# Kernel optimization log

Measured on AMD Instinct MI355X. Metric: run time of the kernel, lower is better.

Reference implementation:

```python
import jax, jax.numpy as jnp
import numpy as np

N = 50000
E = 1600000
IN_DIM = 256
HID = 64
OUT = 16
NEG_SLOPE = 0.01


def setup_inputs() -> dict:
    key = jax.random.key(0)
    ks = jax.random.split(key, 6)
    local_features = jax.random.normal(ks[0], (N, IN_DIM), dtype=jnp.float32)
    edge_index = jax.random.randint(ks[1], (2, E), 0, N, dtype=jnp.int32)
    W0 = jax.random.normal(ks[2], (IN_DIM, HID), dtype=jnp.float32) * 0.05
    a0 = jax.random.normal(ks[3], (2 * HID, 1), dtype=jnp.float32) * 0.05
    W1 = jax.random.normal(ks[4], (HID, OUT), dtype=jnp.float32) * 0.05
    a1 = jax.random.normal(ks[5], (2 * OUT, 1), dtype=jnp.float32) * 0.05
    return {"local_features": local_features, "edge_index": edge_index,
            "W0": W0, "a0": a0, "W1": W1, "a1": a1}


def _segment_softmax(scores, seg, num_segments):
    # softmax over edges sharing the same row (destination) id
    smax = jax.ops.segment_max(scores, seg, num_segments=num_segments)
    ex = jnp.exp(scores - smax[seg])
    ssum = jax.ops.segment_sum(ex, seg, num_segments=num_segments)
    return ex / ssum[seg]


def _gat_layer(H, row, col, W, a, apply_elu):
    d = W.shape[1]
    Hw = H @ W                                   # [N, d]
    # score_e = leaky_relu([Hw[row] || Hw[col]] @ a) = leaky_relu(pr[row] + pc[col])
    pr = Hw @ a[:d, 0]                           # [N]
    pc = Hw @ a[d:, 0]                           # [N]
    s = pr[row] + pc[col]                        # [E]
    s = jnp.where(s >= 0, s, NEG_SLOPE * s)      # leaky_relu
    att = _segment_softmax(s, row, Hw.shape[0])  # per-row sparse softmax (dim=1)
    # out[row] = sum_e att_e * Hw[col_e]
    out = jax.ops.segment_sum(att[:, None] * Hw[col], row, num_segments=Hw.shape[0])
    if apply_elu:
        out = jnp.where(out > 0, out, jnp.expm1(out))  # elu
    return out


def reference(local_features, edge_index, W0, a0, W1, a1):
    row = edge_index[0]
    col = edge_index[1]
    H = _gat_layer(local_features, row, col, W0, a0, apply_elu=True)
    H = _gat_layer(H, row, col, W1, a1, apply_elu=False)
    return jax.nn.log_softmax(H, axis=1)
```

## Files before the change

### kernel.cpp

```cpp
#include <hip/hip_runtime.h>
#include <hip/hip_bf16.h>
#include <math.h>

#define NN 50000
#define NE 1600000
#define BSH 7
#define BCK 391
#define BCAP 5120
#define GEMM_BLKS 98

typedef __attribute__((ext_vector_type(8))) short bf16x8;
typedef __attribute__((ext_vector_type(4))) float f32x4;
typedef __attribute__((ext_vector_type(2))) float f32x2;

__device__ __forceinline__ short f2bf(float f) {
    return (short)((__float_as_uint(f) + 0x8000u) >> 16);
}
__device__ __forceinline__ float lo16(unsigned u) { return __uint_as_float(u << 16); }
__device__ __forceinline__ float hi16(unsigned u) { return __uint_as_float(u & 0xffff0000u); }
__device__ __forceinline__ unsigned enc_f(float f) {
    unsigned u = __float_as_uint(f);
    return (u & 0x80000000u) ? ~u : (u | 0x80000000u);
}
__device__ __forceinline__ float dec_f(unsigned e) {
    return (e & 0x80000000u) ? __uint_as_float(e & 0x7FFFFFFFu)
                             : __uint_as_float(~e);
}

__global__ void __launch_bounds__(1024) gbinA_kernel(
        const float* __restrict__ X,
        const float* __restrict__ W0,
        const float* __restrict__ a,
        __hip_bfloat16* __restrict__ Hwb,
        float* __restrict__ pr,
        float* __restrict__ pc,
        unsigned* __restrict__ max0,
        const int* __restrict__ row, const int* __restrict__ col,
        int* __restrict__ gcursor, unsigned* __restrict__ staging) {
    __shared__ union SH {
        struct {
            unsigned lds_stage[8192];
            unsigned lds_addr[8192];
            int lds_cnt[512];
            int lds_off[512];
            int wg_goff[512];
            int wtot[8];
        } a;
        struct {
            ushort Wt[64 * 264];
            unsigned bmax;
        } g;
    } sh;
    int tid = threadIdx.x;

    if (blockIdx.x < GEMM_BLKS) {
        if (tid == 0) sh.g.bmax = 0u;
        for (int i = tid; i < 16384; i += 1024)
            sh.g.Wt[(i & 63) * 264 + (i >> 6)] = (ushort)f2bf(W0[i]);
        __syncthreads();
        int g256 = tid >> 8, t256 = tid & 255;
        int lane = t256 & 63, wid = t256 >> 6;
        int c = lane & 15, quad = lane >> 4;
        const ushort* wtp[4];
#pragma unroll
        for (int g = 0; g < 4; ++g) wtp[g] = &sh.g.Wt[(g * 16 + c) * 264 + quad * 8];
        float aA[4], aB[4];
#pragma unroll
        for (int g = 0; g < 4; ++g) { aA[g] = a[g * 16 + c]; aB[g] = a[64 + g * 16 + c]; }

        int row0 = blockIdx.x * 512 + g256 * 128 + wid * 16;
        float qmax = -1e30f;

#pragma unroll
        for (int tt = 0; tt < 2; ++tt) {
            int rt = row0 + tt * 64;
            int arow = rt + c; if (arow >= NN) arow = NN - 1;
            const float* xbase = X + (size_t)arow * 256 + quad * 8;
            f32x4 acc[4];
#pragma unroll
            for (int g = 0; g < 4; ++g) acc[g] = (f32x4){0.f, 0.f, 0.f, 0.f};

#pragma unroll
            for (int k0 = 0; k0 < 256; k0 += 32) {
                float4 xa = *(const float4*)(xbase + k0);
                float4 xb = *(const float4*)(xbase + k0 + 4);
                bf16x8 af;
                af[0] = f2bf(xa.x); af[1] = f2bf(xa.y); af[2] = f2bf(xa.z); af[3] = f2bf(xa.w);
                af[4] = f2bf(xb.x); af[5] = f2bf(xb.y); af[6] = f2bf(xb.z); af[7] = f2bf(xb.w);
#pragma unroll
                for (int g = 0; g < 4; ++g) {
                    bf16x8 bg = *(const bf16x8*)(wtp[g] + k0);
                    acc[g] = __builtin_amdgcn_mfma_f32_16x16x32_bf16(af, bg, acc[g], 0, 0, 0);
                }
            }

#pragma unroll
            for (int r = 0; r < 4; ++r) {
                int rr = rt + quad * 4 + r;
                float v0 = acc[0][r], v1 = acc[1][r], v2 = acc[2][r], v3 = acc[3][r];
                if (rr < NN) {
                    __hip_bfloat16* hp = Hwb + (size_t)rr * 64 + c;
                    hp[0]  = __float2bfloat16(v0);
                    hp[16] = __float2bfloat16(v1);
                    hp[32] = __float2bfloat16(v2);
                    hp[48] = __float2bfloat16(v3);
                }
                float pv = v0 * aA[0] + v1 * aA[1] + v2 * aA[2] + v3 * aA[3];
                float qv = v0 * aB[0] + v1 * aB[1] + v2 * aB[2] + v3 * aB[3];
#pragma unroll
                for (int off = 8; off; off >>= 1) {
                    pv += __shfl_xor(pv, off);
                    qv += __shfl_xor(qv, off);
                }
                if (c == 0 && rr < NN) { pr[rr] = pv; pc[rr] = qv; }
                if (rr < NN) qmax = fmaxf(qmax, qv);
            }
        }
        qmax = fmaxf(qmax, __shfl_xor(qmax, 16));
        qmax = fmaxf(qmax, __shfl_xor(qmax, 32));
        if (lane == 0) atomicMax(&sh.g.bmax, enc_f(qmax));
        __syncthreads();
        if (tid == 0) atomicMax(max0, sh.g.bmax);
        return;
    }

    int t = tid;
    int lane = t & 63;
    int w = t >> 6;
    int nbin = gridDim.x - GEMM_BLKS;

    for (int cb = (blockIdx.x - GEMM_BLKS) * 8192; cb < NE; cb += nbin * 8192) {
        int cnt_edges = NE - cb; if (cnt_edges > 8192) cnt_edges = 8192;
        if (t < 512) sh.a.lds_cnt[t] = 0;
        __syncthreads();
        int myb[8]; int mylo[8]; unsigned mypk[8];
        int e0 = cb + t * 8;
        if (t * 8 + 7 < cnt_edges) {
            int4 r0 = *(const int4*)(row + e0);
            int4 r1 = *(const int4*)(row + e0 + 4);
            int4 c0 = *(const int4*)(col + e0);
            int4 c1 = *(const int4*)(col + e0 + 4);
            int rr[8] = {r0.x, r0.y, r0.z, r0.w, r1.x, r1.y, r1.z, r1.w};
            int cc[8] = {c0.x, c0.y, c0.z, c0.w, c1.x, c1.y, c1.z, c1.w};
            #pragma unroll
            for (int i = 0; i < 8; ++i) {
                int b = rr[i] >> BSH;
                myb[i] = b;
                mypk[i] = ((unsigned)(rr[i] & 127) << 16) | (unsigned)cc[i];
                mylo[i] = atomicAdd(&sh.a.lds_cnt[b], 1);
            }
        } else {
            #pragma unroll
            for (int i = 0; i < 8; ++i) {
                int idx = t * 8 + i;
                myb[i] = -1;
                if (idx < cnt_edges) {
                    int e = cb + idx;
                    int r = row[e], c = col[e];
                    myb[i] = r >> BSH;
                    mypk[i] = ((unsigned)(r & 127) << 16) | (unsigned)c;
                    mylo[i] = atomicAdd(&sh.a.lds_cnt[myb[i]], 1);
                }
            }
        }
        __syncthreads();
        int v = (t < 512) ? sh.a.lds_cnt[t] : 0;
        int x = v;
        #pragma unroll
        for (int off = 1; off < 64; off <<= 1) {
            int y = __shfl_up(x, off);
            if (lane >= off) x += y;
        }
        if (t < 512 && lane == 63) sh.a.wtot[w] = x;
        __syncthreads();
        if (t < 8) {
            int s = sh.a.wtot[t];
            #pragma unroll
            for (int off = 1; off < 8; off <<= 1) {
                int y = __shfl_up(s, off, 8);
                if ((t & 7) >= off) s += y;
            }
            sh.a.wtot[t] = s;
        }
        __syncthreads();
        if (t < 512) {
            int add = (w > 0) ? sh.a.wtot[w - 1] : 0;
            sh.a.lds_off[t] = x - v + add;
        }
        if (t < BCK) {
            int cc2 = sh.a.lds_cnt[t];
            sh.a.wg_goff[t] = t * BCAP + (cc2 ? atomicAdd(&gcursor[t], cc2) : 0);
        }
        __syncthreads();
        #pragma unroll
        for (int i = 0; i < 8; ++i) if (myb[i] >= 0) {
            int p = sh.a.lds_off[myb[i]] + mylo[i];
            sh.a.lds_stage[p] = mypk[i];
            sh.a.lds_addr[p] = (unsigned)(sh.a.wg_goff[myb[i]] + mylo[i]);
        }
        __syncthreads();
        for (int i = t; i < cnt_edges; i += 1024)
            staging[sh.a.lds_addr[i]] = sh.a.lds_stage[i];
        __syncthreads();
    }
}

__global__ void __launch_bounds__(1024) binB_kernel(
        const int* __restrict__ gcursor,
        const unsigned* __restrict__ staging,
        int* __restrict__ rowptr,
        ushort* __restrict__ colperm) {
    __shared__ int bsc[512];
    __shared__ int bw[8];
    __shared__ int cur[128];
    __shared__ int wls2[2];
    __shared__ ushort lds_col[BCAP];
    int b = blockIdx.x;
    int t = threadIdx.x;
    int lane = t & 63;
    int w = t >> 6;

    if (t < 512) {
        int v = 0;
        if (t < BCK) {
            v = gcursor[t];
            if (v > BCAP) v = BCAP;
        }
        int x = v;
        #pragma unroll
        for (int off = 1; off < 64; off <<= 1) {
            int y = __shfl_up(x, off);
            if (lane >= off) x += y;
        }
        if (lane == 63) bw[w] = x;
        bsc[t] = x - v;
    }
    __syncthreads();
    if (t < 8) {
        int s = bw[t];
        #pragma unroll
        for (int off = 1; off < 8; off <<= 1) {
            int y = __shfl_up(s, off, 8);
            if ((t & 7) >= off) s += y;
        }
        bw[t] = s;
    }
    __syncthreads();
    int gbase = bsc[b] + ((b >= 64) ? bw[(b >> 6) - 1] : 0);
    int cnt = gcursor[b];
    if (cnt > BCAP) cnt = BCAP;
    if (b == 0 && t == 0) rowptr[NN] = bw[7];
    int rbase = b << BSH;
    int nrows = NN - rbase; if (nrows > 128) nrows = 128;
    const unsigned* sb = staging + (size_t)b * BCAP;

    unsigned ev[8];
    #pragma unroll
    for (int j = 0; j < 2; ++j) {
        int i0 = t * 4 + j * 4096;
        uint4 val = {0u, 0u, 0u, 0u};
        if (i0 + 3 < cnt) {
            val = *(const uint4*)(sb + i0);
        } else {
            if (i0 + 0 < cnt) val.x = sb[i0 + 0];
            if (i0 + 1 < cnt) val.y = sb[i0 + 1];
            if (i0 + 2 < cnt) val.z = sb[i0 + 2];
            if (i0 + 3 < cnt) val.w = sb[i0 + 3];
        }
        ev[j * 4 + 0] = val.x; ev[j * 4 + 1] = val.y;
        ev[j * 4 + 2] = val.z; ev[j * 4 + 3] = val.w;
    }

    if (t < 128) cur[t] = 0;
    __syncthreads();
    #pragma unroll
    for (int j = 0; j < 2; ++j) {
        #pragma unroll
        for (int l = 0; l < 4; ++l) {
            int idx = t * 4 + j * 4096 + l;
            if (idx < cnt) atomicAdd(&cur[ev[j * 4 + l] >> 16], 1);
        }
    }
    __syncthreads();
    int v = 0, x = 0;
    if (t < 128) {
        v = cur[t];
        x = v;
        #pragma unroll
        for (int off = 1; off < 64; off <<= 1) {
            int y = __shfl_up(x, off);
            if (lane >= off) x += y;
        }
        if (lane == 63) wls2[w] = x;
    }
    __syncthreads();
    int excl = 0;
    if (t < 128) {
        excl = x - v + ((w == 1) ? wls2[0] : 0);
        if (t < nrows) rowptr[rbase + t] = gbase + excl;
    }
    __syncthreads();
    if (t < 128) cur[t] = excl;
    __syncthreads();
    #pragma unroll
    for (int j = 0; j < 2; ++j) {
        #pragma unroll
        for (int l = 0; l < 4; ++l) {
            int idx = t * 4 + j * 4096 + l;
            if (idx < cnt) {
                unsigned e = ev[j * 4 + l];
                int pos = atomicAdd(&cur[e >> 16], 1);
                lds_col[pos] = (ushort)(e & 0xFFFFu);
            }
        }
    }
    __syncthreads();
    for (int i = t; i < cnt; i += 1024)
        colperm[gbase + i] = lds_col[i];
}

__global__ void __launch_bounds__(256) node0_kernel(
        const int* __restrict__ rowptr,
        const ushort* __restrict__ colperm,
        const float* __restrict__ pr,
        const float* __restrict__ pc,
        const unsigned* __restrict__ pcmax,
        const ushort* __restrict__ Hwb,
        const float* __restrict__ W1,
        const float* __restrict__ a1,
        __hip_bfloat16* __restrict__ Hw1b,
        float* __restrict__ pr1,
        float* __restrict__ pc1,
        unsigned* __restrict__ max1s) {
    __shared__ float W1s[64 * 17];
    __shared__ float a1s[32];
    __shared__ float hbuf[4][64];
    __shared__ unsigned long long wcbuf[4][64];
    __shared__ unsigned bmax1;
    int t = threadIdx.x;
    if (t == 0) bmax1 = 0u;
    for (int i = t; i < 64 * 16; i += 256)
        W1s[(i >> 4) * 17 + (i & 15)] = W1[i];
    if (t < 32) a1s[t] = a1[t];
    __syncthreads();

    int lane = t & 63;
    int wid = t >> 6;
    int node = blockIdx.x * 4 + wid;
    int k = lane & 15, q = lane >> 4;
    int start = rowptr[node], end = rowptr[node + 1];
    float pri = pr[node];
    float m = pri + dec_f(*pcmax);
    m = (m >= 0.f) ? m : 0.01f * m;

    float wsum = 0.f;
    f32x2 accA = {0.f, 0.f}, accB = {0.f, 0.f};
    for (int base = start; base < end; base += 64) {
        int n = end - base; if (n > 64) n = 64;
        float wv = 0.f; unsigned cv = 0;
        if (lane < n) {
            cv = (unsigned)colperm[base + lane];
            float s = pri + pc[cv];
            s = (s >= 0.f) ? s : 0.01f * s;
            wv = __expf(s - m);
        }
        wsum += wv;
        wcbuf[wid][lane] = ((unsigned long long)cv << 32) |
                           (unsigned long long)__float_as_uint(wv);
        int iters = (n + 3) >> 2;
        #pragma unroll 4
        for (int jj = 0; jj < iters; ++jj) {
            unsigned long long wc = wcbuf[wid][jj * 4 + q];
            float wj = __uint_as_float((unsigned)wc);
            int cj = (int)(wc >> 32);
            uint2 hv = *(const uint2*)(Hwb + (size_t)cj * 64 + k * 4);
            f32x2 wj2 = {wj, wj};
            f32x2 h01 = {lo16(hv.x), hi16(hv.x)};
            f32x2 h23 = {lo16(hv.y), hi16(hv.y)};
            accA += wj2 * h01;
            accB += wj2 * h23;
        }
    }
#pragma unroll
    for (int off = 32; off; off >>= 1) wsum += __shfl_xor(wsum, off);
    float acc0 = accA.x, acc1 = accA.y, acc2 = accB.x, acc3 = accB.y;
    acc0 += __shfl_xor(acc0, 16); acc0 += __shfl_xor(acc0, 32);
    acc1 += __shfl_xor(acc1, 16); acc1 += __shfl_xor(acc1, 32);
    acc2 += __shfl_xor(acc2, 16); acc2 += __shfl_xor(acc2, 32);
    acc3 += __shfl_xor(acc3, 16); acc3 += __shfl_xor(acc3, 32);

    float inv = (wsum > 0.f) ? 1.f / wsum : 0.f;
    float h0 = acc0 * inv; h0 = (h0 > 0.f) ? h0 : (__expf(h0) - 1.f);
    float h1 = acc1 * inv; h1 = (h1 > 0.f) ? h1 : (__expf(h1) - 1.f);
    float h2 = acc2 * inv; h2 = (h2 > 0.f) ? h2 : (__expf(h2) - 1.f);
    float h3 = acc3 * inv; h3 = (h3 > 0.f) ? h3 : (__expf(h3) - 1.f);
    if (q == 0) {
        float4 hh = {h0, h1, h2, h3};
        *(float4*)&hbuf[wid][k * 4] = hh;
    }
    int j = lane & 15, p = lane >> 4;
    const float* hbp = hbuf[wid];
    float vj = 0.f;
#pragma unroll
    for (int i = 0; i < 16; ++i) {
        int kk = p * 16 + i;
        vj = fmaf(hbp[kk], W1s[kk * 17 + j], vj);
    }
    vj += __shfl_xor(vj, 16);
    vj += __shfl_xor(vj, 32);
    if (p == 0) Hw1b[(size_t)node * 16 + j] = __float2bfloat16(vj);
    float pv = vj * a1s[j];
    float qv = vj * a1s[16 + j];
#pragma unroll
    for (int off = 8; off; off >>= 1) {
        pv += __shfl_xor(pv, off);
        qv += __shfl_xor(qv, off);
    }
    if (lane == 0) {
        pr1[node] = pv; pc1[node] = qv;
        atomicMax(&bmax1, enc_f(qv));
    }
    __syncthreads();
    if (t == 0) atomicMax(&max1s[(blockIdx.x & 31) * 16], bmax1);
}

__global__ void __launch_bounds__(256) node1_kernel(
        const int* __restrict__ rowptr,
        const ushort* __restrict__ colperm,
        const float* __restrict__ pr,
        const float* __restrict__ pc,
        const unsigned* __restrict__ max1s,
        const ushort* __restrict__ Hwb,
        float* __restrict__ out) {
    __shared__ unsigned long long wcbuf[4][64];
    __shared__ unsigned gmx;
    int t = threadIdx.x;
    if (t < 32) {
        unsigned v = max1s[t * 16];
        #pragma unroll
        for (int off = 16; off; off >>= 1) {
            unsigned o = (unsigned)__shfl_xor((int)v, off, 32);
            v = (v > o) ? v : o;
        }
        if (t == 0) gmx = v;
    }
    __syncthreads();
    int lane = t & 63;
    int wid = t >> 6;
    int node = blockIdx.x * 4 + wid;
    int k = lane & 3, q = lane >> 2;
    int start = rowptr[node], end = rowptr[node + 1];
    float pri = pr[node];
    float m = pri + dec_f(gmx);
    m = (m >= 0.f) ? m : 0.01f * m;

    float wsum = 0.f;
    f32x2 accA = {0.f, 0.f}, accB = {0.f, 0.f};
    for (int base = start; base < end; base += 64) {
        int n = end - base; if (n > 64) n = 64;
        float wv = 0.f; unsigned cv = 0;
        if (lane < n) {
            cv = (unsigned)colperm[base + lane];
            float s = pri + pc[cv];
            s = (s >= 0.f) ? s : 0.01f * s;
            wv = __expf(s - m);
        }
        wsum += wv;
        wcbuf[wid][lane] = ((unsigned long long)cv << 32) |
                           (unsigned long long)__float_as_uint(wv);
        int iters = (n + 15) >> 4;
        #pragma unroll 4
        for (int jj = 0; jj < iters; ++jj) {
            unsigned long long wc = wcbuf[wid][jj * 16 + q];
            float wj = __uint_as_float((unsigned)wc);
            int cj = (int)(wc >> 32);
            uint2 hv = *(const uint2*)(Hwb + (size_t)cj * 16 + k * 4);
            f32x2 wj2 = {wj, wj};
            accA += wj2 * (f32x2){lo16(hv.x), hi16(hv.x)};
            accB += wj2 * (f32x2){lo16(hv.y), hi16(hv.y)};
        }
    }
#pragma unroll
    for (int off = 32; off; off >>= 1) wsum += __shfl_xor(wsum, off);
    float ac[4] = {accA.x, accA.y, accB.x, accB.y};
#pragma unroll
    for (int j4 = 0; j4 < 4; ++j4) {
        ac[j4] += __shfl_xor(ac[j4], 4);
        ac[j4] += __shfl_xor(ac[j4], 8);
        ac[j4] += __shfl_xor(ac[j4], 16);
        ac[j4] += __shfl_xor(ac[j4], 32);
    }
    float inv = (wsum > 0.f) ? 1.f / wsum : 0.f;
    float v0 = ac[0] * inv, v1 = ac[1] * inv;
    float v2 = ac[2] * inv, v3 = ac[3] * inv;
    float mm = fmaxf(fmaxf(v0, v1), fmaxf(v2, v3));
    mm = fmaxf(mm, __shfl_xor(mm, 1, 4));
    mm = fmaxf(mm, __shfl_xor(mm, 2, 4));
    float ssx = __expf(v0 - mm) + __expf(v1 - mm) + __expf(v2 - mm) + __expf(v3 - mm);
    ssx += __shfl_xor(ssx, 1, 4);
    ssx += __shfl_xor(ssx, 2, 4);
    float lse = mm + __logf(ssx);
    if (q == 0) {
        float4 o = {v0 - lse, v1 - lse, v2 - lse, v3 - lse};
        *(float4*)(out + (size_t)node * 16 + k * 4) = o;
    }
}

extern "C" void kernel_launch(void* const* d_in, const int* in_sizes, int n_in,
                              void* d_out, int out_size, void* d_ws, size_t ws_size,
                              hipStream_t stream) {
    const float* X  = (const float*)d_in[0];
    const int*   ei = (const int*)d_in[1];
    const float* W0 = (const float*)d_in[2];
    const float* a0 = (const float*)d_in[3];
    const float* W1 = (const float*)d_in[4];
    const float* a1 = (const float*)d_in[5];
    float* out = (float*)d_out;

    const int* row = ei;
    const int* col = ei + NE;

    char* wsb = (char*)d_ws;
    size_t off = 0;
    auto alloc = [&](size_t bytes) {
        void* p = wsb + off;
        off += (bytes + 15) & ~(size_t)15;
        return p;
    };
    unsigned* maxes = (unsigned*)alloc(16);
    unsigned* max1s = (unsigned*)alloc(512 * 4);
    int* gcursor    = (int*)alloc(512 * 4);
    size_t zinit = off;
    int* rowptr     = (int*)alloc((NN + 2) * 4);
    unsigned* staging = (unsigned*)alloc((size_t)BCK * BCAP * 4);
    ushort* colperm = (ushort*)alloc((size_t)NE * 2);
    __hip_bfloat16* Hw0b = (__hip_bfloat16*)alloc((size_t)NN * 64 * 2);
    float* pr0      = (float*)alloc(NN * 4);
    float* pc0      = (float*)alloc(NN * 4);
    __hip_bfloat16* Hw1b = (__hip_bfloat16*)alloc((size_t)NN * 16 * 2);
    float* pr1      = (float*)alloc(NN * 4);
    float* pc1      = (float*)alloc(NN * 4);

    hipMemsetAsync(wsb, 0, zinit, stream);

    gbinA_kernel<<<GEMM_BLKS + 196, 1024, 0, stream>>>(X, W0, a0, Hw0b, pr0, pc0,
                                                       &maxes[0], row, col,
                                                       gcursor, staging);
    binB_kernel<<<BCK, 1024, 0, stream>>>(gcursor, staging, rowptr, colperm);

    node0_kernel<<<NN / 4, 256, 0, stream>>>(rowptr, colperm, pr0, pc0,
                                             &maxes[0], (const ushort*)Hw0b,
                                             W1, a1, Hw1b, pr1, pc1, max1s);

    node1_kernel<<<NN / 4, 256, 0, stream>>>(rowptr, colperm, pr1, pc1,
                                             max1s, (const ushort*)Hw1b, out);
}
```

Measured before the change: 206.0 us.

## Split layer-0 aggregation into two column-range passes for cache locality

Edges in each row are binned by whether their column index falls below or above a split point, and a mid pointer per row is recorded. Layer-0 aggregation is split into two kernels, each gathering features from only half the node range, so the gathered working set is smaller and more cache-resident. Partial accumulators and weight sums from the first pass go through a large global buffer that the second pass reads back. This adds a full extra launch plus substantial extra memory traffic for the intermediate accumulators.

```diff
diff --git a/kernel.cpp b/kernel.cpp
--- a/kernel.cpp
+++ b/kernel.cpp
@@ -8,6 +8,7 @@
 #define BCK 391
 #define BCAP 5120
 #define GEMM_BLKS 98
+#define COLSPLIT 25000
 
 typedef __attribute__((ext_vector_type(8))) short bf16x8;
 typedef __attribute__((ext_vector_type(4))) float f32x4;
@@ -209,11 +210,12 @@
         const int* __restrict__ gcursor,
         const unsigned* __restrict__ staging,
         int* __restrict__ rowptr,
+        int* __restrict__ midptr,
         ushort* __restrict__ colperm) {
     __shared__ int bsc[512];
     __shared__ int bw[8];
-    __shared__ int cur[128];
-    __shared__ int wls2[2];
+    __shared__ int cur[256];
+    __shared__ int wls4[4];
     __shared__ ushort lds_col[BCAP];
     int b = blockIdx.x;
     int t = threadIdx.x;
@@ -271,36 +273,7 @@
         ev[j * 4 + 2] = val.z; ev[j * 4 + 3] = val.w;
     }
 
-    if (t < 128) cur[t] = 0;
-    __syncthreads();
-    #pragma unroll
-    for (int j = 0; j < 2; ++j) {
-        #pragma unroll
-        for (int l = 0; l < 4; ++l) {
-            int idx = t * 4 + j * 4096 + l;
-            if (idx < cnt) atomicAdd(&cur[ev[j * 4 + l] >> 16], 1);
-        }
-    }
-    __syncthreads();
-    int v = 0, x = 0;
-    if (t < 128) {
-        v = cur[t];
-        x = v;
-        #pragma unroll
-        for (int off = 1; off < 64; off <<= 1) {
-            int y = __shfl_up(x, off);
-            if (lane >= off) x += y;
-        }
-        if (lane == 63) wls2[w] = x;
-    }
-    __syncthreads();
-    int excl = 0;
-    if (t < 128) {
-        excl = x - v + ((w == 1) ? wls2[0] : 0);
-        if (t < nrows) rowptr[rbase + t] = gbase + excl;
-    }
-    __syncthreads();
-    if (t < 128) cur[t] = excl;
+    if (t < 256) cur[t] = 0;
     __syncthreads();
     #pragma unroll
     for (int j = 0; j < 2; ++j) {
@@ -309,7 +282,51 @@
             int idx = t * 4 + j * 4096 + l;
             if (idx < cnt) {
                 unsigned e = ev[j * 4 + l];
-                int pos = atomicAdd(&cur[e >> 16], 1);
+                int bin = (int)((e >> 16) << 1) | (int)((e & 0xffffu) >= COLSPLIT);
+                atomicAdd(&cur[bin], 1);
+            }
+        }
+    }
+    __syncthreads();
+    int v = 0, x = 0;
+    if (t < 256) {
+        v = cur[t];
+        x = v;
+        #pragma unroll
+        for (int off = 1; off < 64; off <<= 1) {
+            int y = __shfl_up(x, off);
+            if (lane >= off) x += y;
+        }
+        if (lane == 63) wls4[w] = x;
+    }
+    __syncthreads();
+    if (t == 0) {
+        int s = 0;
+        #pragma unroll
+        for (int i = 0; i < 4; ++i) { int tv = wls4[i]; wls4[i] = s; s += tv; }
+    }
+    __syncthreads();
+    int excl = 0;
+    if (t < 256) {
+        excl = x - v + wls4[w];
+        int r = t >> 1;
+        if (r < nrows) {
+            if ((t & 1) == 0) rowptr[rbase + r] = gbase + excl;
+            else              midptr[rbase + r] = gbase + excl;
+        }
+    }
+    __syncthreads();
+    if (t < 256) cur[t] = excl;
+    __syncthreads();
+    #pragma unroll
+    for (int j = 0; j < 2; ++j) {
+        #pragma unroll
+        for (int l = 0; l < 4; ++l) {
+            int idx = t * 4 + j * 4096 + l;
+            if (idx < cnt) {
+                unsigned e = ev[j * 4 + l];
+                int bin = (int)((e >> 16) << 1) | (int)((e & 0xffffu) >= COLSPLIT);
+                int pos = atomicAdd(&cur[bin], 1);
                 lds_col[pos] = (ushort)(e & 0xFFFFu);
             }
         }
@@ -319,13 +336,71 @@
         colperm[gbase + i] = lds_col[i];
 }
 
-__global__ void __launch_bounds__(256) node0_kernel(
+__global__ void __launch_bounds__(256) node0a_kernel(
         const int* __restrict__ rowptr,
+        const int* __restrict__ midptr,
         const ushort* __restrict__ colperm,
         const float* __restrict__ pr,
         const float* __restrict__ pc,
         const unsigned* __restrict__ pcmax,
         const ushort* __restrict__ Hwb,
+        float* __restrict__ accbuf,
+        float* __restrict__ wsumA) {
+    __shared__ unsigned long long wcbuf[4][64];
+    int t = threadIdx.x;
+    int lane = t & 63;
+    int wid = t >> 6;
+    int node = blockIdx.x * 4 + wid;
+    int k = lane & 15, q = lane >> 4;
+    int start = rowptr[node], end = midptr[node];
+    float pri = pr[node];
+    float m = pri + dec_f(*pcmax);
+    m = (m >= 0.f) ? m : 0.01f * m;
+
+    float wsum = 0.f;
+    f32x2 accA = {0.f, 0.f}, accB = {0.f, 0.f};
+    for (int base = start; base < end; base += 64) {
+        int n = end - base; if (n > 64) n = 64;
+        float wv = 0.f; unsigned cv = 0;
+        if (lane < n) {
+            cv = (unsigned)colperm[base + lane];
+            float s = pri + pc[cv];
+            s = (s >= 0.f) ? s : 0.01f * s;
+            wv = __expf(s - m);
+        }
+        wsum += wv;
+        wcbuf[wid][lane] = ((unsigned long long)cv << 32) |
+                           (unsigned long long)__float_as_uint(wv);
+        int iters = (n + 3) >> 2;
+        #pragma unroll 4
+        for (int jj = 0; jj < iters; ++jj) {
+            unsigned long long wc = wcbuf[wid][jj * 4 + q];
+            float wj = __uint_as_float((unsigned)wc);
+            int cj = (int)(wc >> 32);
+            uint2 hv = *(const uint2*)(Hwb + (size_t)cj * 64 + k * 4);
+            f32x2 wj2 = {wj, wj};
+            accA += wj2 * (f32x2){lo16(hv.x), hi16(hv.x)};
+            accB += wj2 * (f32x2){lo16(hv.y), hi16(hv.y)};
+        }
+    }
+#pragma unroll
+    for (int off = 32; off; off >>= 1) wsum += __shfl_xor(wsum, off);
+    if (lane == 0) wsumA[node] = wsum;
+    f32x4 av = {accA.x, accA.y, accB.x, accB.y};
+    __builtin_nontemporal_store(av,
+        (f32x4*)(accbuf + ((size_t)node << 8) + lane * 4));
+}
+
+__global__ void __launch_bounds__(256) node0b_kernel(
+        const int* __restrict__ rowptr,
+        const int* __restrict__ midptr,
+        const ushort* __restrict__ colperm,
+        const float* __restrict__ pr,
+        const float* __restrict__ pc,
+        const unsigned* __restrict__ pcmax,
+        const ushort* __restrict__ Hwb,
+        const float* __restrict__ accbuf,
+        const float* __restrict__ wsumA,
         const float* __restrict__ W1,
         const float* __restrict__ a1,
         __hip_bfloat16* __restrict__ Hw1b,
@@ -348,13 +423,15 @@
     int wid = t >> 6;
     int node = blockIdx.x * 4 + wid;
     int k = lane & 15, q = lane >> 4;
-    int start = rowptr[node], end = rowptr[node + 1];
+    int start = midptr[node], end = rowptr[node + 1];
     float pri = pr[node];
     float m = pri + dec_f(*pcmax);
     m = (m >= 0.f) ? m : 0.01f * m;
 
+    f32x4 av = __builtin_nontemporal_load(
+        (const f32x4*)(accbuf + ((size_t)node << 8) + lane * 4));
+    f32x2 accA = {av.x, av.y}, accB = {av.z, av.w};
     float wsum = 0.f;
-    f32x2 accA = {0.f, 0.f}, accB = {0.f, 0.f};
     for (int base = start; base < end; base += 64) {
         int n = end - base; if (n > 64) n = 64;
         float wv = 0.f; unsigned cv = 0;
@@ -375,14 +452,13 @@
             int cj = (int)(wc >> 32);
             uint2 hv = *(const uint2*)(Hwb + (size_t)cj * 64 + k * 4);
             f32x2 wj2 = {wj, wj};
-            f32x2 h01 = {lo16(hv.x), hi16(hv.x)};
-            f32x2 h23 = {lo16(hv.y), hi16(hv.y)};
-            accA += wj2 * h01;
-            accB += wj2 * h23;
+            accA += wj2 * (f32x2){lo16(hv.x), hi16(hv.x)};
+            accB += wj2 * (f32x2){lo16(hv.y), hi16(hv.y)};
         }
     }
 #pragma unroll
     for (int off = 32; off; off >>= 1) wsum += __shfl_xor(wsum, off);
+    wsum += wsumA[node];
     float acc0 = accA.x, acc1 = accA.y, acc2 = accB.x, acc3 = accB.y;
     acc0 += __shfl_xor(acc0, 16); acc0 += __shfl_xor(acc0, 32);
     acc1 += __shfl_xor(acc1, 16); acc1 += __shfl_xor(acc1, 32);
@@ -532,6 +608,7 @@
     int* gcursor    = (int*)alloc(512 * 4);
     size_t zinit = off;
     int* rowptr     = (int*)alloc((NN + 2) * 4);
+    int* midptr     = (int*)alloc((NN + 2) * 4);
     unsigned* staging = (unsigned*)alloc((size_t)BCK * BCAP * 4);
     ushort* colperm = (ushort*)alloc((size_t)NE * 2);
     __hip_bfloat16* Hw0b = (__hip_bfloat16*)alloc((size_t)NN * 64 * 2);
@@ -540,17 +617,23 @@
     __hip_bfloat16* Hw1b = (__hip_bfloat16*)alloc((size_t)NN * 16 * 2);
     float* pr1      = (float*)alloc(NN * 4);
     float* pc1      = (float*)alloc(NN * 4);
+    float* accbuf   = (float*)alloc((size_t)NN * 256 * 4);
+    float* wsumA    = (float*)alloc(NN * 4);
 
     hipMemsetAsync(wsb, 0, zinit, stream);
 
     gbinA_kernel<<<GEMM_BLKS + 196, 1024, 0, stream>>>(X, W0, a0, Hw0b, pr0, pc0,
                                                        &maxes[0], row, col,
                                                        gcursor, staging);
-    binB_kernel<<<BCK, 1024, 0, stream>>>(gcursor, staging, rowptr, colperm);
-
-    node0_kernel<<<NN / 4, 256, 0, stream>>>(rowptr, colperm, pr0, pc0,
-                                             &maxes[0], (const ushort*)Hw0b,
-                                             W1, a1, Hw1b, pr1, pc1, max1s);
+    binB_kernel<<<BCK, 1024, 0, stream>>>(gcursor, staging, rowptr, midptr, colperm);
+
+    node0a_kernel<<<NN / 4, 256, 0, stream>>>(rowptr, midptr, colperm, pr0, pc0,
+                                              &maxes[0], (const ushort*)Hw0b,
+                                              accbuf, wsumA);
+    node0b_kernel<<<NN / 4, 256, 0, stream>>>(rowptr, midptr, colperm, pr0, pc0,
+                                              &maxes[0], (const ushort*)Hw0b,
+                                              accbuf, wsumA,
+                                              W1, a1, Hw1b, pr1, pc1, max1s);
 
     node1_kernel<<<NN / 4, 256, 0, stream>>>(rowptr, colperm, pr1, pc1,
                                              max1s, (const ushort*)Hw1b, out);
```

Result: slower. 229.7 us (+11.5%).

## Precompute layer-0 attention weights during CSR binning and pack with column ids

Applied to the files above, without the earlier changes.

The layer-0 edge attention weights (leaky-relu plus exp against the global bound) are now computed in the binning kernel and stored as fp16 next to the column index in a 32-bit packed CSR array. node0 then streams these packed entries directly, with no pc gather, no exp and no LDS staging, in a single flat loop. node1 reads the column from the upper 16 bits. This doubles the size of the column array and computes the weights in fp16, which can lose precision or underflow for small weights.

```diff
diff --git a/kernel.cpp b/kernel.cpp
--- a/kernel.cpp
+++ b/kernel.cpp
@@ -1,5 +1,6 @@
 #include <hip/hip_runtime.h>
 #include <hip/hip_bf16.h>
+#include <hip/hip_fp16.h>
 #include <math.h>
 
 #define NN 50000
@@ -208,13 +209,18 @@
 __global__ void __launch_bounds__(1024) binB_kernel(
         const int* __restrict__ gcursor,
         const unsigned* __restrict__ staging,
+        const float* __restrict__ pr0,
+        const float* __restrict__ pc0,
+        const unsigned* __restrict__ pcmax,
         int* __restrict__ rowptr,
-        ushort* __restrict__ colperm) {
+        unsigned* __restrict__ colperm2) {
     __shared__ int bsc[512];
     __shared__ int bw[8];
     __shared__ int cur[128];
     __shared__ int wls2[2];
-    __shared__ ushort lds_col[BCAP];
+    __shared__ float pr_l[128];
+    __shared__ float m_l[128];
+    __shared__ unsigned lds_colw[BCAP];
     int b = blockIdx.x;
     int t = threadIdx.x;
     int lane = t & 63;
@@ -253,6 +259,16 @@
     int rbase = b << BSH;
     int nrows = NN - rbase; if (nrows > 128) nrows = 128;
     const unsigned* sb = staging + (size_t)b * BCAP;
+    float pcm = dec_f(*pcmax);
+
+    if (t < 128) {
+        int r = rbase + t;
+        float pri = (r < NN) ? pr0[r] : 0.f;
+        float mm = pri + pcm;
+        mm = (mm >= 0.f) ? mm : 0.01f * mm;
+        pr_l[t] = pri;
+        m_l[t] = mm;
+    }
 
     unsigned ev[8];
     #pragma unroll
@@ -271,6 +287,17 @@
         ev[j * 4 + 2] = val.z; ev[j * 4 + 3] = val.w;
     }
 
+    float pcv[8];
+    #pragma unroll
+    for (int j = 0; j < 2; ++j) {
+        #pragma unroll
+        for (int l = 0; l < 4; ++l) {
+            int idx = t * 4 + j * 4096 + l;
+            int c = (idx < cnt) ? (int)(ev[j * 4 + l] & 0xffffu) : 0;
+            pcv[j * 4 + l] = pc0[c];
+        }
+    }
+
     if (t < 128) cur[t] = 0;
     __syncthreads();
     #pragma unroll
@@ -309,22 +336,24 @@
             int idx = t * 4 + j * 4096 + l;
             if (idx < cnt) {
                 unsigned e = ev[j * 4 + l];
-                int pos = atomicAdd(&cur[e >> 16], 1);
-                lds_col[pos] = (ushort)(e & 0xFFFFu);
+                int lr = (int)(e >> 16);
+                float s = pr_l[lr] + pcv[j * 4 + l];
+                s = (s >= 0.f) ? s : 0.01f * s;
+                float wv = __expf(s - m_l[lr]);
+                unsigned short w16 = __half_as_ushort(__float2half(wv));
+                int pos = atomicAdd(&cur[lr], 1);
+                lds_colw[pos] = ((e & 0xffffu) << 16) | (unsigned)w16;
             }
         }
     }
     __syncthreads();
     for (int i = t; i < cnt; i += 1024)
-        colperm[gbase + i] = lds_col[i];
+        colperm2[gbase + i] = lds_colw[i];
 }
 
 __global__ void __launch_bounds__(256) node0_kernel(
         const int* __restrict__ rowptr,
-        const ushort* __restrict__ colperm,
-        const float* __restrict__ pr,
-        const float* __restrict__ pc,
-        const unsigned* __restrict__ pcmax,
+        const unsigned* __restrict__ colperm2,
         const ushort* __restrict__ Hwb,
         const float* __restrict__ W1,
         const float* __restrict__ a1,
@@ -335,7 +364,6 @@
     __shared__ float W1s[64 * 17];
     __shared__ float a1s[32];
     __shared__ float hbuf[4][64];
-    __shared__ unsigned long long wcbuf[4][64];
     __shared__ unsigned bmax1;
     int t = threadIdx.x;
     if (t == 0) bmax1 = 0u;
@@ -349,40 +377,27 @@
     int node = blockIdx.x * 4 + wid;
     int k = lane & 15, q = lane >> 4;
     int start = rowptr[node], end = rowptr[node + 1];
-    float pri = pr[node];
-    float m = pri + dec_f(*pcmax);
-    m = (m >= 0.f) ? m : 0.01f * m;
+    int iters = (end - start + 3) >> 2;
 
     float wsum = 0.f;
     f32x2 accA = {0.f, 0.f}, accB = {0.f, 0.f};
-    for (int base = start; base < end; base += 64) {
-        int n = end - base; if (n > 64) n = 64;
-        float wv = 0.f; unsigned cv = 0;
-        if (lane < n) {
-            cv = (unsigned)colperm[base + lane];
-            float s = pri + pc[cv];
-            s = (s >= 0.f) ? s : 0.01f * s;
-            wv = __expf(s - m);
-        }
-        wsum += wv;
-        wcbuf[wid][lane] = ((unsigned long long)cv << 32) |
-                           (unsigned long long)__float_as_uint(wv);
-        int iters = (n + 3) >> 2;
-        #pragma unroll 4
-        for (int jj = 0; jj < iters; ++jj) {
-            unsigned long long wc = wcbuf[wid][jj * 4 + q];
-            float wj = __uint_as_float((unsigned)wc);
-            int cj = (int)(wc >> 32);
-            uint2 hv = *(const uint2*)(Hwb + (size_t)cj * 64 + k * 4);
-            f32x2 wj2 = {wj, wj};
-            f32x2 h01 = {lo16(hv.x), hi16(hv.x)};
-            f32x2 h23 = {lo16(hv.y), hi16(hv.y)};
-            accA += wj2 * h01;
-            accB += wj2 * h23;
-        }
-    }
-#pragma unroll
-    for (int off = 32; off; off >>= 1) wsum += __shfl_xor(wsum, off);
+    int e = start + q;
+    const ushort* hb = Hwb + k * 4;
+    #pragma unroll 4
+    for (int jj = 0; jj < iters; ++jj, e += 4) {
+        int idx = (e < end) ? e : start;
+        unsigned ew = colperm2[idx];
+        float wj = __half2float(__ushort_as_half((unsigned short)(ew & 0xffffu)));
+        wj = (e < end) ? wj : 0.f;
+        int cj = (int)(ew >> 16);
+        uint2 hv = *(const uint2*)(hb + (size_t)cj * 64);
+        wsum += wj;
+        f32x2 wj2 = {wj, wj};
+        accA += wj2 * (f32x2){lo16(hv.x), hi16(hv.x)};
+        accB += wj2 * (f32x2){lo16(hv.y), hi16(hv.y)};
+    }
+    wsum += __shfl_xor(wsum, 16);
+    wsum += __shfl_xor(wsum, 32);
     float acc0 = accA.x, acc1 = accA.y, acc2 = accB.x, acc3 = accB.y;
     acc0 += __shfl_xor(acc0, 16); acc0 += __shfl_xor(acc0, 32);
     acc1 += __shfl_xor(acc1, 16); acc1 += __shfl_xor(acc1, 32);
@@ -426,7 +441,7 @@
 
 __global__ void __launch_bounds__(256) node1_kernel(
         const int* __restrict__ rowptr,
-        const ushort* __restrict__ colperm,
+        const unsigned* __restrict__ colperm2,
         const float* __restrict__ pr,
         const float* __restrict__ pc,
         const unsigned* __restrict__ max1s,
@@ -460,7 +475,7 @@
         int n = end - base; if (n > 64) n = 64;
         float wv = 0.f; unsigned cv = 0;
         if (lane < n) {
-            cv = (unsigned)colperm[base + lane];
+            cv = colperm2[base + lane] >> 16;
             float s = pri + pc[cv];
             s = (s >= 0.f) ? s : 0.01f * s;
             wv = __expf(s - m);
@@ -533,7 +548,7 @@
     size_t zinit = off;
     int* rowptr     = (int*)alloc((NN + 2) * 4);
     unsigned* staging = (unsigned*)alloc((size_t)BCK * BCAP * 4);
-    ushort* colperm = (ushort*)alloc((size_t)NE * 2);
+    unsigned* colperm2 = (unsigned*)alloc((size_t)NE * 4);
     __hip_bfloat16* Hw0b = (__hip_bfloat16*)alloc((size_t)NN * 64 * 2);
     float* pr0      = (float*)alloc(NN * 4);
     float* pc0      = (float*)alloc(NN * 4);
@@ -546,12 +561,13 @@
     gbinA_kernel<<<GEMM_BLKS + 196, 1024, 0, stream>>>(X, W0, a0, Hw0b, pr0, pc0,
                                                        &maxes[0], row, col,
                                                        gcursor, staging);
-    binB_kernel<<<BCK, 1024, 0, stream>>>(gcursor, staging, rowptr, colperm);
-
-    node0_kernel<<<NN / 4, 256, 0, stream>>>(rowptr, colperm, pr0, pc0,
-                                             &maxes[0], (const ushort*)Hw0b,
+    binB_kernel<<<BCK, 1024, 0, stream>>>(gcursor, staging, pr0, pc0, &maxes[0],
+                                          rowptr, colperm2);
+
+    node0_kernel<<<NN / 4, 256, 0, stream>>>(rowptr, colperm2,
+                                             (const ushort*)Hw0b,
                                              W1, a1, Hw1b, pr1, pc1, max1s);
 
-    node1_kernel<<<NN / 4, 256, 0, stream>>>(rowptr, colperm, pr1, pc1,
+    node1_kernel<<<NN / 4, 256, 0, stream>>>(rowptr, colperm2, pr1, pc1,
                                              max1s, (const ushort*)Hw1b, out);
 }
```

Measured after the change: 212.6 us. 3.2% more time.
